# Kernel tuning notes

Hardware: AMD Instinct MI355X
Metric: run time of the kernel (lower is better)

Reference implementation:

```python
import math
import jax, jax.numpy as jnp
import numpy as np

NUM_HEADS = 16
NUM_LANDMARKS = 64
INV_ITERS = 6
ATT_SIZE = 1024
HEAD_SIZE = ATT_SIZE // NUM_HEADS  # dk = 64
NEG = -100000.0


def moore_penrose_pinv(x, num_iter):
    # lucidrains-style iterative Moore-Penrose pseudo-inverse
    abs_x = jnp.abs(x)
    col = abs_x.sum(axis=-1)
    row = abs_x.sum(axis=-2)
    z = jnp.swapaxes(x, -1, -2) / (jnp.max(col) * jnp.max(row))
    I = jnp.eye(x.shape[-1], dtype=x.dtype)
    for _ in range(num_iter):
        xz = x @ z
        z = 0.25 * z @ (13.0 * I - xz @ (15.0 * I - xz @ (7.0 * I - xz)))
    return z


def masked_softmax_scores(k, q, mask):
    # q @ k^T (dk=1: q already scaled) + mask, softmax over last dim
    s = jnp.einsum('bhmd,bhld->bhml', q, k)
    if mask is not None:
        s = s + (1.0 - mask) * NEG
    return jax.nn.softmax(s, axis=-1)


def setup_inputs() -> dict:
    key = jax.random.key(0)
    k1, k2, k3 = jax.random.split(key, 3)
    B, L, D = 4, 4096, 1024
    x = jax.random.normal(k1, (B, L, D), dtype=jnp.float32)
    attention_mask = jnp.ones((B, L), dtype=jnp.float32)
    w_kqv = jax.random.normal(k2, (3 * ATT_SIZE, D), dtype=jnp.float32) * 0.02
    w_out = jax.random.normal(k3, (ATT_SIZE, ATT_SIZE), dtype=jnp.float32) * 0.02
    b_out = jnp.zeros((ATT_SIZE,), dtype=jnp.float32)
    return {"x": x, "attention_mask": attention_mask,
            "w_kqv": w_kqv, "w_out": w_out, "b_out": b_out}


def reference(x, attention_mask, w_kqv, w_out, b_out):
    B, L, D = x.shape
    H, nl, hd = NUM_HEADS, NUM_LANDMARKS, HEAD_SIZE
    seg = L // nl  # landmark segment length (L already a multiple of nl)

    kqv = x @ w_kqv.T  # [B, L, 3A]
    k, q, v = jnp.split(kqv, 3, axis=-1)
    split = lambda t: t.reshape(B, L, H, hd).transpose(0, 2, 1, 3)  # [B,H,L,hd]
    k, q, v = split(k), split(q), split(v)

    mask = attention_mask[:, None, :]  # [B,1,L]
    denom = mask.reshape(B, 1, nl, seg).sum(-1) + 1e-08  # [B,1,nl]
    mask_lm = (denom > 0).astype(x.dtype)  # [B,1,nl]
    denom4 = denom[..., None]              # [B,1,nl,1]
    maskL = mask[..., None]                # [B,1,L,1]

    q = q * maskL
    k = k * maskL
    v = v * maskL

    s1_mask = maskL * mask_lm[..., None, :]               # [B,1,L,nl]
    s2_mask = mask_lm[..., None] * mask_lm[..., None, :]  # [B,1,nl,nl]
    s3_mask = jnp.swapaxes(s1_mask, -1, -2)               # [B,1,nl,L]

    q = q / math.sqrt(HEAD_SIZE)
    q_lm = q.reshape(B, H, nl, seg, hd).sum(-2) / denom4  # [B,H,nl,hd]
    k_lm = k.reshape(B, H, nl, seg, hd).sum(-2) / denom4

    scores_1 = masked_softmax_scores(k_lm, q, s1_mask)     # [B,H,L,nl]
    scores_2 = masked_softmax_scores(k_lm, q_lm, s2_mask)  # [B,H,nl,nl]
    scores_3 = masked_softmax_scores(k, q_lm, s3_mask)     # [B,H,nl,L]

    z_star = moore_penrose_pinv(scores_2, INV_ITERS)       # [B,H,nl,nl]
    out = scores_1 @ (z_star @ (scores_3 @ v))             # [B,H,L,hd]

    out = out.transpose(0, 2, 1, 3).reshape(B, L, H * hd)  # merge heads
    return out @ w_out.T + b_out
```

## Files before the change

kernel.cpp:

```cpp
#include <hip/hip_runtime.h>
#include <hip/hip_bf16.h>


static constexpr int Bn  = 4;
static constexpr int Ln  = 4096;
static constexpr int Dn  = 1024;
static constexpr int Hn  = 16;
static constexpr int HDn = 64;
static constexpr int NLn = 64;
static constexpr int SEGn = 64;
static constexpr int BHn = Bn * Hn;
static constexpr int Mn  = Bn * Ln;
static constexpr int NCH = 8;
#define NEG_BIG (-100000.0f)

static constexpr size_t OFF_KT  = 0;
static constexpr size_t OFF_QT  = 16777216;
static constexpr size_t OFF_VT  = 33554432;
static constexpr size_t OFF_WOH = 33554432;
static constexpr size_t OFF_WH  = 50331648;
static constexpr size_t OFF_QLM = 50331648;
static constexpr size_t OFF_KLM = 50593792;
static constexpr size_t OFF_S2  = 50855936;
static constexpr size_t OFF_Z   = 51118080;
static constexpr size_t OFF_WM  = 51380224;
static constexpr size_t OFF_PM  = 51642368;
static constexpr size_t OFF_PS  = 51675136;
static constexpr size_t OFF_GM  = 51707904;
static constexpr size_t OFF_XS  = 53477376;
static constexpr size_t OFF_PO  = 53477376;

using bf16x8 = __attribute__((ext_vector_type(8))) short;
using f32x16 = __attribute__((ext_vector_type(16))) float;
using s16x4  = __attribute__((ext_vector_type(4))) short;

__device__ __forceinline__ unsigned short f2bf(float f) {
    unsigned int u = __float_as_uint(f);
    return (unsigned short)((u + 0x7fffu + ((u >> 16) & 1u)) >> 16);
}
__device__ __forceinline__ float bf2f(unsigned short h) {
    return __uint_as_float((unsigned int)h << 16);
}
__device__ __forceinline__ void cvt8s(const float* fs, bf16x8& hv, bf16x8& lv) {
    #pragma unroll
    for (int e = 0; e < 8; ++e) {
        const unsigned int u = __float_as_uint(fs[e]);
        const unsigned short h = (unsigned short)(u >> 16);
        hv[e] = (short)h;
        lv[e] = (short)f2bf(fs[e] - bf2f(h));
    }
}
typedef __attribute__((address_space(1))) void gvoid;
typedef __attribute__((address_space(3))) void lvoid;
__device__ __forceinline__ void async16(void* l, const void* g) {
    __builtin_amdgcn_global_load_lds((gvoid*)(size_t)g, (lvoid*)l, 16, 0, 0);
}

__global__ __launch_bounds__(256) void k_pack(
    const float* __restrict__ src, unsigned short* __restrict__ dh, int row0)
{
    __shared__ float Ls[128][33];
    const int rt = blockIdx.x, kt = blockIdx.y;
    const int tid = threadIdx.x;
    #pragma unroll
    for (int p = 0; p < 4; ++p) {
        const int row = p * 32 + (tid >> 3);
        const int c4 = (tid & 7) * 4;
        const float4 v = *(const float4*)&src[(size_t)(row0 + rt * 128 + row) * 1024 + kt * 32 + c4];
        Ls[row][c4 + 0] = v.x; Ls[row][c4 + 1] = v.y;
        Ls[row][c4 + 2] = v.z; Ls[row][c4 + 3] = v.w;
    }
    __syncthreads();
    const size_t tb = (size_t)(rt * 32 + kt) * 4096;
    for (int s = tid; s < 512; s += 256) {
        const int g = s >> 7, kk = (s >> 6) & 1, l = s & 63;
        const int row = g * 32 + (l & 31);
        const int k0 = kk * 16 + ((l >> 5) & 1) * 8;
        bf16x8 hv;
        #pragma unroll
        for (int e = 0; e < 8; ++e) hv[e] = (short)f2bf(Ls[row][k0 + e]);
        *(bf16x8*)&dh[tb + s * 8] = hv;
    }
}

#define GEMM4W_CORE(A_, B_, NNB)                                               \
    __shared__ __attribute__((aligned(16))) char smem[16384];                  \
    const int tid = threadIdx.x;                                               \
    const int lane = tid & 63, wid = tid >> 6;                                 \
    const int cpx = gridDim.x >> 3;                                            \
    const int wg = (blockIdx.x & 7) * cpx + (blockIdx.x >> 3);                 \
    const int bm = wg / (NNB), bn = wg % (NNB);                                \
    const int wrow = wid >> 1, wcol = wid & 1;                                 \
    const unsigned short* gsrc =                                               \
        (wid < 2 ? (A_) + (size_t)bm * 131072 : (B_) + (size_t)bn * 131072)    \
        + (wid & 1) * 2048 + lane * 8;                                         \
    char* ldst = smem + wid * 4096;                                            \
    f32x16 acc[2][2] = {};                                                     \
    for (int kt = 0; kt < 32; ++kt) {                                          \
        const unsigned short* g = gsrc + (size_t)kt * 4096;                    \
        __syncthreads();                                                       \
        _Pragma("unroll")                                                      \
        for (int i = 0; i < 4; ++i)                                            \
            async16(ldst + i * 1024, g + i * 512);                             \
        __syncthreads();                                                       \
        _Pragma("unroll")                                                      \
        for (int kk = 0; kk < 2; ++kk) {                                       \
            bf16x8 fa[2], fb[2];                                               \
            _Pragma("unroll")                                                  \
            for (int ti = 0; ti < 2; ++ti) {                                   \
                const int o = (((wrow * 2 + ti) * 2 + kk) << 10) + lane * 16;  \
                fa[ti] = *(const bf16x8*)(smem + o);                           \
            }                                                                  \
            _Pragma("unroll")                                                  \
            for (int tj = 0; tj < 2; ++tj) {                                   \
                const int o = (((wcol * 2 + tj) * 2 + kk) << 10) + lane * 16;  \
                fb[tj] = *(const bf16x8*)(smem + 8192 + o);                    \
            }                                                                  \
            _Pragma("unroll")                                                  \
            for (int ti = 0; ti < 2; ++ti)                                     \
                _Pragma("unroll")                                              \
                for (int tj = 0; tj < 2; ++tj)                                 \
                    acc[ti][tj] = __builtin_amdgcn_mfma_f32_32x32x16_bf16(     \
                        fa[ti], fb[tj], acc[ti][tj], 0, 0, 0);                 \
        }                                                                      \
    }

__global__ __launch_bounds__(256) void k_kqv_gemm(
    const unsigned short* __restrict__ xh,
    const unsigned short* __restrict__ wh,
    const float* __restrict__ mask,
    float* __restrict__ Kt, float* __restrict__ Qt, float* __restrict__ Vt,
    int row0)
{
    GEMM4W_CORE(xh, wh, 24)
    const int part = bn >> 3;
    #pragma unroll
    for (int ti = 0; ti < 2; ++ti) {
        #pragma unroll
        for (int tj = 0; tj < 2; ++tj) {
            const int col = (bn * 128 + wcol * 64 + tj * 32 + (lane & 31)) & 1023;
            const int h = col >> 6, d = col & 63;
            #pragma unroll
            for (int r = 0; r < 16; ++r) {
                const int row = row0 + bm * 128 + wrow * 64 + ti * 32
                              + (r & 3) + 8 * (r >> 2) + 4 * (lane >> 5);
                const int b = row >> 12, l = row & 4095;
                const float mk = mask[b * Ln + l];
                const size_t idx = ((size_t)(b * Hn + h) * Ln + l) * HDn + d;
                const float v = acc[ti][tj][r] * mk;
                if (part == 0)      Kt[idx] = v;
                else if (part == 1) Qt[idx] = v * 0.125f;
                else                Vt[idx] = v;
            }
        }
    }
}

__global__ __launch_bounds__(256) void k_out_gemm(
    const unsigned short* __restrict__ ah_,
    const unsigned short* __restrict__ bh_,
    const float* __restrict__ bias, float* __restrict__ out)
{
    GEMM4W_CORE(ah_, bh_, 8)
    #pragma unroll
    for (int ti = 0; ti < 2; ++ti) {
        #pragma unroll
        for (int tj = 0; tj < 2; ++tj) {
            const int col = bn * 128 + wcol * 64 + tj * 32 + (lane & 31);
            const float bb = bias[col];
            #pragma unroll
            for (int r = 0; r < 16; ++r) {
                const int row = bm * 128 + wrow * 64 + ti * 32
                              + (r & 3) + 8 * (r >> 2) + 4 * (lane >> 5);
                out[(size_t)row * Dn + col] = acc[ti][tj][r] + bb;
            }
        }
    }
}

__global__ __launch_bounds__(64) void k_landmarks(
    const float* __restrict__ Kt, const float* __restrict__ Qt,
    const float* __restrict__ mask,
    float* __restrict__ klm, float* __restrict__ qlm, int* __restrict__ gmax)
{
    const int blk = blockIdx.x;
    const int m = blk & 63, bh = blk >> 6, b = bh >> 4;
    const int d = threadIdx.x;
    if (blk == 0 && d < 2) gmax[d] = 0;
    float mv = mask[b * Ln + m * SEGn + d];
    #pragma unroll
    for (int off = 32; off; off >>= 1) mv += __shfl_down(mv, off);
    const float denom = __shfl(mv, 0) + 1e-8f;
    const float* kp = Kt + ((size_t)bh * Ln + m * SEGn) * HDn + d;
    const float* qp = Qt + ((size_t)bh * Ln + m * SEGn) * HDn + d;
    float sk = 0.f, sq = 0.f;
    for (int j = 0; j < SEGn; ++j) {
        sk += kp[(size_t)j * HDn];
        sq += qp[(size_t)j * HDn];
    }
    klm[((size_t)bh * NLn + m) * HDn + d] = sk / denom;
    qlm[((size_t)bh * NLn + m) * HDn + d] = sq / denom;
}

__global__ __launch_bounds__(64) void k_s2(
    const float* __restrict__ qlm, const float* __restrict__ klm,
    float* __restrict__ s2, int* __restrict__ gmax)
{
    const int bh = blockIdx.x;
    __shared__ float ql[64][65];
    __shared__ float kl[64][65];
    __shared__ float sr[64][65];
    const int t = threadIdx.x;
    for (int idx = t; idx < 4096; idx += 64) {
        ql[idx >> 6][idx & 63] = qlm[(size_t)bh * 4096 + idx];
        kl[idx >> 6][idx & 63] = klm[(size_t)bh * 4096 + idx];
    }
    __syncthreads();
    float mx = -1e30f;
    for (int mp = 0; mp < 64; ++mp) {
        float s = 0.f;
        #pragma unroll 8
        for (int d2 = 0; d2 < 64; ++d2) s = fmaf(ql[t][d2], kl[mp][d2], s);
        sr[t][mp] = s;
        mx = fmaxf(mx, s);
    }
    float sum = 0.f;
    for (int mp = 0; mp < 64; ++mp) {
        const float e = expf(sr[t][mp] - mx);
        sr[t][mp] = e;
        sum += e;
    }
    const float inv = 1.f / sum;
    float rs = 0.f;
    for (int mp = 0; mp < 64; ++mp) {
        const float v = sr[t][mp] * inv;
        sr[t][mp] = v;
        s2[(size_t)bh * 4096 + t * 64 + mp] = v;
        rs += fabsf(v);
    }
    __syncthreads();
    float cs = 0.f;
    for (int mm = 0; mm < 64; ++mm) cs += fabsf(sr[mm][t]);
    float rmax = rs, cmax = cs;
    #pragma unroll
    for (int off = 32; off; off >>= 1) {
        rmax = fmaxf(rmax, __shfl_down(rmax, off));
        cmax = fmaxf(cmax, __shfl_down(cmax, off));
    }
    if (t == 0) {
        atomicMax(&gmax[0], __float_as_int(rmax));
        atomicMax(&gmax[1], __float_as_int(cmax));
    }
}

template<int SUB>
__device__ __forceinline__ void mm64v(
    float* C, int ldc, const float* Ag, int lda,
    const float* Bm, int ldb, float dg, float scl)
{
    const int tid = threadIdx.x;
    const int tx = tid & 15, ty = tid >> 4;
    const int i0 = ty << 2, j0 = tx << 2;
    float acc[4][4] = {};
    for (int k0 = 0; k0 < 64; k0 += 4) {
        float4 a4[4], b4[4];
        #pragma unroll
        for (int i = 0; i < 4; ++i)
            a4[i] = *(const float4*)&Ag[(size_t)(i0 + i) * lda + k0];
        #pragma unroll
        for (int kk = 0; kk < 4; ++kk)
            b4[kk] = *(const float4*)&Bm[(size_t)(k0 + kk) * ldb + j0];
        if (SUB) {
            #pragma unroll
            for (int kk = 0; kk < 4; ++kk) {
                float* bp = (float*)&b4[kk];
                #pragma unroll
                for (int j = 0; j < 4; ++j)
                    bp[j] = ((k0 + kk == j0 + j) ? dg : 0.0f) - bp[j];
            }
        }
        #pragma unroll
        for (int i = 0; i < 4; ++i) {
            const float* ap = (const float*)&a4[i];
            #pragma unroll
            for (int kk = 0; kk < 4; ++kk) {
                const float* bp = (const float*)&b4[kk];
                #pragma unroll
                for (int j = 0; j < 4; ++j)
                    acc[i][j] = fmaf(ap[kk], bp[j], acc[i][j]);
            }
        }
    }
    __syncthreads();
    #pragma unroll
    for (int i = 0; i < 4; ++i)
        #pragma unroll
        for (int j = 0; j < 4; ++j) C[(size_t)(i0 + i) * ldc + j0 + j] = scl * acc[i][j];
    __syncthreads();
}

__global__ __launch_bounds__(256) void k_pinv(
    const float* __restrict__ s2, const int* __restrict__ gmax,
    float* __restrict__ zout)
{
    __shared__ float Zb[64][68];
    __shared__ float XZ[64][68];
    __shared__ float Tb[64][68];
    const int bh = blockIdx.x;
    const int tid = threadIdx.x;
    const float* X = s2 + (size_t)bh * 4096;
    const float scale = 1.0f / (__int_as_float(gmax[0]) * __int_as_float(gmax[1]));
    for (int idx = tid; idx < 4096; idx += 256) {
        const int i = idx >> 6, j = idx & 63;
        Zb[i][j] = X[j * 64 + i] * scale;
    }
    __syncthreads();
    for (int it = 0; it < 6; ++it) {
        mm64v<0>(&XZ[0][0], 68, X, 64, &Zb[0][0], 68, 0.f, 1.f);
        mm64v<1>(&Tb[0][0], 68, &XZ[0][0], 68, &XZ[0][0], 68, 7.f, 1.f);
        mm64v<1>(&Tb[0][0], 68, &XZ[0][0], 68, &Tb[0][0], 68, 15.f, 1.f);
        mm64v<1>(&Zb[0][0], 68, &Zb[0][0], 68, &Tb[0][0], 68, 13.f, 0.25f);
    }
    for (int idx = tid; idx < 4096; idx += 256)
        zout[(size_t)bh * 4096 + idx] = Zb[idx >> 6][idx & 63];
}

__global__ __launch_bounds__(256) void k_s3v_part(
    const float* __restrict__ qlm, const float* __restrict__ Kt,
    const float* __restrict__ Vt, const float* __restrict__ mask,
    float* __restrict__ Opart, float* __restrict__ mpart, float* __restrict__ spart)
{
    __shared__ float Sm[64][65];
    __shared__ float Ks[64][65];
    __shared__ float Vs[64][65];
    __shared__ unsigned short Qp[2][4096];
    __shared__ float red[64][4], red2[64][4];
    __shared__ float rowmax[64], rowsum[64], fac[64], mrow[64];
    const int bh = blockIdx.x, ch = blockIdx.y;
    const int b = bh >> 4;
    const int tid = threadIdx.x;
    const int lane = tid & 63, wid = tid >> 6;
    const int wr = wid >> 1, wc = wid & 1;

    for (int idx = tid; idx < 4096; idx += 256)
        Sm[idx >> 6][idx & 63] = qlm[(size_t)bh * 4096 + idx];
    if (tid < 64) { rowmax[tid] = -1e30f; rowsum[tid] = 0.f; }
    __syncthreads();
    for (int s = tid; s < 512; s += 256) {
        const int g = s >> 8, kc = (s >> 6) & 3, l = s & 63;
        const int row = g * 32 + (l & 31);
        const int k0 = kc * 16 + ((l >> 5) & 1) * 8;
        bf16x8 hv, lv;
        cvt8s(&Sm[row][k0], hv, lv);
        *(bf16x8*)&Qp[0][s * 8] = hv;
        *(bf16x8*)&Qp[1][s * 8] = lv;
    }
    f32x16 accO = {};
    const int t0beg = ch * (Ln / NCH), t0end = t0beg + (Ln / NCH);
    for (int t0 = t0beg; t0 < t0end; t0 += 64) {
        __syncthreads();
        for (int idx = tid; idx < 4096; idx += 256) {
            const int r = idx >> 6, c2 = idx & 63;
            Ks[r][c2] = Kt[((size_t)bh * Ln + t0 + r) * HDn + c2];
            Vs[r][c2] = Vt[((size_t)bh * Ln + t0 + r) * HDn + c2];
        }
        if (tid < 64) mrow[tid] = mask[b * Ln + t0 + tid];
        __syncthreads();
        f32x16 acc = {};
        #pragma unroll
        for (int kc = 0; kc < 4; ++kc) {
            const bf16x8 a_h = *(const bf16x8*)&Qp[0][((wr * 4 + kc) * 64 + lane) * 8];
            const bf16x8 a_l = *(const bf16x8*)&Qp[1][((wr * 4 + kc) * 64 + lane) * 8];
            const int brow = wc * 32 + (lane & 31);
            const int k0 = kc * 16 + (lane >> 5) * 8;
            bf16x8 b_h, b_l;
            cvt8s(&Ks[brow][k0], b_h, b_l);
            acc = __builtin_amdgcn_mfma_f32_32x32x16_bf16(a_h, b_h, acc, 0, 0, 0);
            acc = __builtin_amdgcn_mfma_f32_32x32x16_bf16(a_h, b_l, acc, 0, 0, 0);
            acc = __builtin_amdgcn_mfma_f32_32x32x16_bf16(a_l, b_h, acc, 0, 0, 0);
        }
        #pragma unroll
        for (int r = 0; r < 16; ++r) {
            const int row = wr * 32 + (r & 3) + 8 * (r >> 2) + 4 * (lane >> 5);
            const int col = wc * 32 + (lane & 31);
            Sm[row][col] = acc[r] + (1.f - mrow[col]) * NEG_BIG;
        }
        __syncthreads();
        {
            const int row = tid >> 2, sg = tid & 3, c0 = sg * 16;
            float mx = -1e30f;
            #pragma unroll
            for (int c = 0; c < 16; ++c) mx = fmaxf(mx, Sm[row][c0 + c]);
            red[row][sg] = mx;
            __syncthreads();
            const float nm = fmaxf(rowmax[row],
                fmaxf(fmaxf(red[row][0], red[row][1]), fmaxf(red[row][2], red[row][3])));
            const float f = __expf(rowmax[row] - nm);
            float ps = 0.f;
            #pragma unroll
            for (int c = 0; c < 16; ++c) {
                const float e = __expf(Sm[row][c0 + c] - nm);
                Sm[row][c0 + c] = e;
                ps += e;
            }
            red2[row][sg] = ps;
            __syncthreads();
            if (sg == 0) {
                rowsum[row] = rowsum[row] * f
                    + red2[row][0] + red2[row][1] + red2[row][2] + red2[row][3];
                rowmax[row] = nm;
                fac[row] = f;
            }
        }
        __syncthreads();
        #pragma unroll
        for (int r = 0; r < 16; ++r) {
            const int row = wr * 32 + (r & 3) + 8 * (r >> 2) + 4 * (lane >> 5);
            accO[r] *= fac[row];
        }
        #pragma unroll
        for (int kc = 0; kc < 4; ++kc) {
            const int arow = wr * 32 + (lane & 31);
            const int ak0 = kc * 16 + (lane >> 5) * 8;
            bf16x8 a_h, a_l;
            cvt8s(&Sm[arow][ak0], a_h, a_l);
            const int bcol = wc * 32 + (lane & 31);
            const int bk0 = kc * 16 + (lane >> 5) * 8;
            float bw[8];
            #pragma unroll
            for (int e = 0; e < 8; ++e) bw[e] = Vs[bk0 + e][bcol];
            bf16x8 b_h, b_l;
            cvt8s(bw, b_h, b_l);
            accO = __builtin_amdgcn_mfma_f32_32x32x16_bf16(a_h, b_h, accO, 0, 0, 0);
            accO = __builtin_amdgcn_mfma_f32_32x32x16_bf16(a_h, b_l, accO, 0, 0, 0);
            accO = __builtin_amdgcn_mfma_f32_32x32x16_bf16(a_l, b_h, accO, 0, 0, 0);
        }
    }
    __syncthreads();
    #pragma unroll
    for (int r = 0; r < 16; ++r) {
        const int row = wr * 32 + (r & 3) + 8 * (r >> 2) + 4 * (lane >> 5);
        Vs[row][wc * 32 + (lane & 31)] = accO[r];
    }
    __syncthreads();
    const size_t ob = (size_t)(bh * NCH + ch) * 4096;
    for (int idx = tid; idx < 4096; idx += 256)
        Opart[ob + idx] = Vs[idx >> 6][idx & 63];
    if (tid < 64) {
        mpart[(bh * NCH + ch) * 64 + tid] = rowmax[tid];
        spart[(bh * NCH + ch) * 64 + tid] = rowsum[tid];
    }
}

__global__ __launch_bounds__(256) void k_mergez(
    const float* __restrict__ Opart, const float* __restrict__ mpart,
    const float* __restrict__ spart, const float* __restrict__ Zs,
    float* __restrict__ Wm)
{
    __shared__ float Sv[64][68];
    __shared__ float Zb[64][68];
    const int bh = blockIdx.x, tid = threadIdx.x;
    for (int idx = tid; idx < 4096; idx += 256)
        Zb[idx >> 6][idx & 63] = Zs[(size_t)bh * 4096 + idx];
    {
        const int r = tid >> 2, c0 = (tid & 3) * 16;
        float e[NCH];
        float M = -1e30f;
        #pragma unroll
        for (int c = 0; c < NCH; ++c) {
            e[c] = mpart[(bh * NCH + c) * 64 + r];
            M = fmaxf(M, e[c]);
        }
        float S = 0.f;
        #pragma unroll
        for (int c = 0; c < NCH; ++c) {
            e[c] = expf(e[c] - M);
            S += spart[(bh * NCH + c) * 64 + r] * e[c];
        }
        const float invS = 1.f / S;
        for (int col = c0; col < c0 + 16; ++col) {
            float o = 0.f;
            #pragma unroll
            for (int c = 0; c < NCH; ++c)
                o += Opart[(size_t)(bh * NCH + c) * 4096 + r * 64 + col] * e[c];
            Sv[r][col] = o * invS;
        }
    }
    __syncthreads();
    const int tx = tid & 15, ty = tid >> 4;
    const int i0 = ty << 2, j0 = tx << 2;
    float acc[4][4] = {};
    for (int k0 = 0; k0 < 64; k0 += 4) {
        float4 a4[4], b4[4];
        #pragma unroll
        for (int i = 0; i < 4; ++i)
            a4[i] = *(const float4*)&Zb[i0 + i][k0];
        #pragma unroll
        for (int kk = 0; kk < 4; ++kk)
            b4[kk] = *(const float4*)&Sv[k0 + kk][j0];
        #pragma unroll
        for (int i = 0; i < 4; ++i) {
            const float* ap = (const float*)&a4[i];
            #pragma unroll
            for (int kk = 0; kk < 4; ++kk) {
                const float* bp = (const float*)&b4[kk];
                #pragma unroll
                for (int j = 0; j < 4; ++j)
                    acc[i][j] = fmaf(ap[kk], bp[j], acc[i][j]);
            }
        }
    }
    #pragma unroll
    for (int i = 0; i < 4; ++i)
        #pragma unroll
        for (int j = 0; j < 4; ++j)
            Wm[(size_t)bh * 4096 + (i0 + i) * 64 + j0 + j] = acc[i][j];
}

__global__ __launch_bounds__(256) void k_attn_out(
    const float* __restrict__ Qt, const float* __restrict__ klm,
    const float* __restrict__ Wm, unsigned short* __restrict__ ah)
{
    const int lt = blockIdx.x;
    const int bh = blockIdx.y;
    const int b = bh >> 4, h = bh & 15;
    __shared__ float Sm[64][65];
    __shared__ float Ks[64][65];
    __shared__ float Ws[64][65];
    __shared__ unsigned short Qp[2][4096];
    __shared__ float red[64][4], red2[64][4];
    __shared__ float invr[64];
    const int tid = threadIdx.x;
    const int lane = tid & 63, wid = tid >> 6;
    const int wr = wid >> 1, wc = wid & 1;

    for (int idx = tid; idx < 4096; idx += 256) {
        const int r = idx >> 6, c2 = idx & 63;
        Sm[r][c2] = Qt[((size_t)bh * Ln + lt * 64 + r) * HDn + c2];
        Ks[r][c2] = klm[(size_t)bh * 4096 + idx];
        Ws[r][c2] = Wm[(size_t)bh * 4096 + idx];
    }
    __syncthreads();
    for (int s = tid; s < 512; s += 256) {
        const int g = s >> 8, kc = (s >> 6) & 3, l = s & 63;
        const int row = g * 32 + (l & 31);
        const int k0 = kc * 16 + ((l >> 5) & 1) * 8;
        bf16x8 hv, lv;
        cvt8s(&Sm[row][k0], hv, lv);
        *(bf16x8*)&Qp[0][s * 8] = hv;
        *(bf16x8*)&Qp[1][s * 8] = lv;
    }
    __syncthreads();
    f32x16 acc = {};
    #pragma unroll
    for (int kc = 0; kc < 4; ++kc) {
        const bf16x8 a_h = *(const bf16x8*)&Qp[0][((wr * 4 + kc) * 64 + lane) * 8];
        const bf16x8 a_l = *(const bf16x8*)&Qp[1][((wr * 4 + kc) * 64 + lane) * 8];
        const int brow = wc * 32 + (lane & 31);
        const int k0 = kc * 16 + (lane >> 5) * 8;
        bf16x8 b_h, b_l;
        cvt8s(&Ks[brow][k0], b_h, b_l);
        acc = __builtin_amdgcn_mfma_f32_32x32x16_bf16(a_h, b_h, acc, 0, 0, 0);
        acc = __builtin_amdgcn_mfma_f32_32x32x16_bf16(a_h, b_l, acc, 0, 0, 0);
        acc = __builtin_amdgcn_mfma_f32_32x32x16_bf16(a_l, b_h, acc, 0, 0, 0);
    }
    #pragma unroll
    for (int r = 0; r < 16; ++r) {
        const int row = wr * 32 + (r & 3) + 8 * (r >> 2) + 4 * (lane >> 5);
        Sm[row][wc * 32 + (lane & 31)] = acc[r];
    }
    __syncthreads();
    {
        const int row = tid >> 2, sg = tid & 3, c0 = sg * 16;
        float mx = -1e30f;
        #pragma unroll
        for (int c = 0; c < 16; ++c) mx = fmaxf(mx, Sm[row][c0 + c]);
        red[row][sg] = mx;
        __syncthreads();
        mx = fmaxf(fmaxf(red[row][0], red[row][1]), fmaxf(red[row][2], red[row][3]));
        float ps = 0.f;
        #pragma unroll
        for (int c = 0; c < 16; ++c) {
            const float e = __expf(Sm[row][c0 + c] - mx);
            Sm[row][c0 + c] = e;
            ps += e;
        }
        red2[row][sg] = ps;
        __syncthreads();
        if (sg == 0)
            invr[row] = 1.f / (red2[row][0] + red2[row][1] + red2[row][2] + red2[row][3]);
    }
    __syncthreads();
    f32x16 acc2 = {};
    #pragma unroll
    for (int kc = 0; kc < 4; ++kc) {
        const int arow = wr * 32 + (lane & 31);
        const int ak0 = kc * 16 + (lane >> 5) * 8;
        bf16x8 a_h, a_l;
        cvt8s(&Sm[arow][ak0], a_h, a_l);
        const int bcol = wc * 32 + (lane & 31);
        const int bk0 = kc * 16 + (lane >> 5) * 8;
        float bw[8];
        #pragma unroll
        for (int e = 0; e < 8; ++e) bw[e] = Ws[bk0 + e][bcol];
        bf16x8 b_h, b_l;
        cvt8s(bw, b_h, b_l);
        acc2 = __builtin_amdgcn_mfma_f32_32x32x16_bf16(a_h, b_h, acc2, 0, 0, 0);
        acc2 = __builtin_amdgcn_mfma_f32_32x32x16_bf16(a_h, b_l, acc2, 0, 0, 0);
        acc2 = __builtin_amdgcn_mfma_f32_32x32x16_bf16(a_l, b_h, acc2, 0, 0, 0);
    }
    __syncthreads();
    #pragma unroll
    for (int r = 0; r < 16; ++r) {
        const int row = wr * 32 + (r & 3) + 8 * (r >> 2) + 4 * (lane >> 5);
        Ks[row][wc * 32 + (lane & 31)] = acc2[r];
    }
    __syncthreads();
    const int tx = tid & 15, ty = tid >> 4;
    const int i0 = ty << 2, j0 = tx << 2;
    const int kd = h * 64 + j0;
    const int kt2 = kd >> 5, kc2 = kd & 31;
    const int kk2 = kc2 >> 4, half = (kc2 & 15) >> 3, e0 = kc2 & 7;
    #pragma unroll
    for (int i = 0; i < 4; ++i) {
        const float inv = invr[i0 + i];
        const int gm = b * Ln + lt * 64 + i0 + i;
        const int mt = gm >> 7, g2 = (gm & 127) >> 5, lrow = gm & 31;
        const size_t u = (size_t)(mt * 32 + kt2) * 4096
                       + (size_t)(((g2 * 2 + kk2) * 64 + half * 32 + lrow) * 8 + e0);
        s16x4 hv;
        #pragma unroll
        for (int j = 0; j < 4; ++j)
            hv[j] = (short)f2bf(Ks[i0 + i][j0 + j] * inv);
        *(s16x4*)&ah[u] = hv;
    }
}

extern "C" void kernel_launch(void* const* d_in, const int* in_sizes, int n_in,
                              void* d_out, int out_size, void* d_ws, size_t ws_size,
                              hipStream_t stream)
{
    (void)in_sizes; (void)n_in; (void)out_size;
    const float* x    = (const float*)d_in[0];
    const float* mask = (const float*)d_in[1];
    const float* wkqv = (const float*)d_in[2];
    const float* wout = (const float*)d_in[3];
    const float* bout = (const float*)d_in[4];
    float* out = (float*)d_out;
    float* ws  = (float*)d_ws;

    float* Kt   = ws + OFF_KT;
    float* Qt   = ws + OFF_QT;
    float* Vt   = ws + OFF_VT;
    float* qlm  = ws + OFF_QLM;
    float* klm  = ws + OFF_KLM;
    float* s2   = ws + OFF_S2;
    float* zst  = ws + OFF_Z;
    float* Wm   = ws + OFF_WM;
    int*   gmax = (int*)(ws + OFF_GM);
    float* mpart = ws + OFF_PM;
    float* spart = ws + OFF_PS;
    float* Opart = ws + OFF_PO;
    unsigned short* wh  = (unsigned short*)(ws + OFF_WH);
    unsigned short* woh = (unsigned short*)(ws + OFF_WOH);
    unsigned short* attn_h = (unsigned short*)(ws + OFF_KT);

    int S = 2048;
    if (ws_size >= (size_t)(OFF_XS + 8192 * 512) * 4) S = 8192;
    else if (ws_size >= (size_t)(OFF_XS + 2097152) * 4) S = 4096;
    unsigned short* xhs = (unsigned short*)(ws + OFF_XS);

    k_pack<<<dim3(24, 32), 256, 0, stream>>>(wkqv, wh, 0);
    for (int s = 0; s < Mn / S; ++s) {
        k_pack<<<dim3(S / 128, 32), 256, 0, stream>>>(x, xhs, s * S);
        k_kqv_gemm<<<(S / 128) * 24, 256, 0, stream>>>(
            xhs, wh, mask, Kt, Qt, Vt, s * S);
    }
    k_landmarks<<<BHn * NLn, 64, 0, stream>>>(Kt, Qt, mask, klm, qlm, gmax);
    k_s2<<<BHn, 64, 0, stream>>>(qlm, klm, s2, gmax);
    k_pinv<<<BHn, 256, 0, stream>>>(s2, gmax, zst);
    k_s3v_part<<<dim3(BHn, NCH), 256, 0, stream>>>(qlm, Kt, Vt, mask, Opart, mpart, spart);
    k_pack<<<dim3(8, 32), 256, 0, stream>>>(wout, woh, 0);
    k_mergez<<<BHn, 256, 0, stream>>>(Opart, mpart, spart, zst, Wm);
    k_attn_out<<<dim3(Ln / 64, BHn), 256, 0, stream>>>(Qt, klm, Wm, attn_h);
    k_out_gemm<<<128 * 8, 256, 0, stream>>>(attn_h, woh, bout, out);
}
```

Baseline: 461.1 us.

## Drop split-bf16 correction MFMAs, widen pinv to 512 threads, enlarge pack chunk

Replaces the three-MFMA hi/lo split-bf16 products in the s3v and attention-output kernels with a single rounded-bf16 MFMA, which removes two thirds of that matrix work and the low-part conversions and LDS staging. The pinv kernel now runs 512 threads per block, each computing a 2x4 tile instead of 4x4, to add parallelism to the serial Newton iterations. The x pack/GEMM chunk grows to 16384 rows when the workspace allows, cutting launches. Dropping the correction terms lowers accuracy in the softmax-weighted products.

```diff
diff --git a/kernel.cpp b/kernel.cpp
--- a/kernel.cpp
+++ b/kernel.cpp
@@ -38,17 +38,9 @@
     unsigned int u = __float_as_uint(f);
     return (unsigned short)((u + 0x7fffu + ((u >> 16) & 1u)) >> 16);
 }
-__device__ __forceinline__ float bf2f(unsigned short h) {
-    return __uint_as_float((unsigned int)h << 16);
-}
-__device__ __forceinline__ void cvt8s(const float* fs, bf16x8& hv, bf16x8& lv) {
-    #pragma unroll
-    for (int e = 0; e < 8; ++e) {
-        const unsigned int u = __float_as_uint(fs[e]);
-        const unsigned short h = (unsigned short)(u >> 16);
-        hv[e] = (short)h;
-        lv[e] = (short)f2bf(fs[e] - bf2f(h));
-    }
+__device__ __forceinline__ void cvt8r(const float* fs, bf16x8& hv) {
+    #pragma unroll
+    for (int e = 0; e < 8; ++e) hv[e] = (short)f2bf(fs[e]);
 }
 typedef __attribute__((address_space(1))) void gvoid;
 typedef __attribute__((address_space(3))) void lvoid;
@@ -77,8 +69,7 @@
         const int row = g * 32 + (l & 31);
         const int k0 = kk * 16 + ((l >> 5) & 1) * 8;
         bf16x8 hv;
-        #pragma unroll
-        for (int e = 0; e < 8; ++e) hv[e] = (short)f2bf(Ls[row][k0 + e]);
+        cvt8r(&Ls[row][k0], hv);
         *(bf16x8*)&dh[tb + s * 8] = hv;
     }
 }
@@ -254,18 +245,18 @@
 }
 
 template<int SUB>
-__device__ __forceinline__ void mm64v(
+__device__ __forceinline__ void mm64v512(
     float* C, int ldc, const float* Ag, int lda,
     const float* Bm, int ldb, float dg, float scl)
 {
     const int tid = threadIdx.x;
     const int tx = tid & 15, ty = tid >> 4;
-    const int i0 = ty << 2, j0 = tx << 2;
-    float acc[4][4] = {};
+    const int i0 = ty << 1, j0 = tx << 2;
+    float acc[2][4] = {};
     for (int k0 = 0; k0 < 64; k0 += 4) {
-        float4 a4[4], b4[4];
-        #pragma unroll
-        for (int i = 0; i < 4; ++i)
+        float4 a4[2], b4[4];
+        #pragma unroll
+        for (int i = 0; i < 2; ++i)
             a4[i] = *(const float4*)&Ag[(size_t)(i0 + i) * lda + k0];
         #pragma unroll
         for (int kk = 0; kk < 4; ++kk)
@@ -280,7 +271,7 @@
             }
         }
         #pragma unroll
-        for (int i = 0; i < 4; ++i) {
+        for (int i = 0; i < 2; ++i) {
             const float* ap = (const float*)&a4[i];
             #pragma unroll
             for (int kk = 0; kk < 4; ++kk) {
@@ -293,13 +284,13 @@
     }
     __syncthreads();
     #pragma unroll
-    for (int i = 0; i < 4; ++i)
+    for (int i = 0; i < 2; ++i)
         #pragma unroll
         for (int j = 0; j < 4; ++j) C[(size_t)(i0 + i) * ldc + j0 + j] = scl * acc[i][j];
     __syncthreads();
 }
 
-__global__ __launch_bounds__(256) void k_pinv(
+__global__ __launch_bounds__(512) void k_pinv(
     const float* __restrict__ s2, const int* __restrict__ gmax,
     float* __restrict__ zout)
 {
@@ -310,18 +301,18 @@
     const int tid = threadIdx.x;
     const float* X = s2 + (size_t)bh * 4096;
     const float scale = 1.0f / (__int_as_float(gmax[0]) * __int_as_float(gmax[1]));
-    for (int idx = tid; idx < 4096; idx += 256) {
+    for (int idx = tid; idx < 4096; idx += 512) {
         const int i = idx >> 6, j = idx & 63;
         Zb[i][j] = X[j * 64 + i] * scale;
     }
     __syncthreads();
     for (int it = 0; it < 6; ++it) {
-        mm64v<0>(&XZ[0][0], 68, X, 64, &Zb[0][0], 68, 0.f, 1.f);
-        mm64v<1>(&Tb[0][0], 68, &XZ[0][0], 68, &XZ[0][0], 68, 7.f, 1.f);
-        mm64v<1>(&Tb[0][0], 68, &XZ[0][0], 68, &Tb[0][0], 68, 15.f, 1.f);
-        mm64v<1>(&Zb[0][0], 68, &Zb[0][0], 68, &Tb[0][0], 68, 13.f, 0.25f);
-    }
-    for (int idx = tid; idx < 4096; idx += 256)
+        mm64v512<0>(&XZ[0][0], 68, X, 64, &Zb[0][0], 68, 0.f, 1.f);
+        mm64v512<1>(&Tb[0][0], 68, &XZ[0][0], 68, &XZ[0][0], 68, 7.f, 1.f);
+        mm64v512<1>(&Tb[0][0], 68, &XZ[0][0], 68, &Tb[0][0], 68, 15.f, 1.f);
+        mm64v512<1>(&Zb[0][0], 68, &Zb[0][0], 68, &Tb[0][0], 68, 13.f, 0.25f);
+    }
+    for (int idx = tid; idx < 4096; idx += 512)
         zout[(size_t)bh * 4096 + idx] = Zb[idx >> 6][idx & 63];
 }
 
@@ -333,7 +324,7 @@
     __shared__ float Sm[64][65];
     __shared__ float Ks[64][65];
     __shared__ float Vs[64][65];
-    __shared__ unsigned short Qp[2][4096];
+    __shared__ unsigned short Qp[4096];
     __shared__ float red[64][4], red2[64][4];
     __shared__ float rowmax[64], rowsum[64], fac[64], mrow[64];
     const int bh = blockIdx.x, ch = blockIdx.y;
@@ -350,10 +341,9 @@
         const int g = s >> 8, kc = (s >> 6) & 3, l = s & 63;
         const int row = g * 32 + (l & 31);
         const int k0 = kc * 16 + ((l >> 5) & 1) * 8;
-        bf16x8 hv, lv;
-        cvt8s(&Sm[row][k0], hv, lv);
-        *(bf16x8*)&Qp[0][s * 8] = hv;
-        *(bf16x8*)&Qp[1][s * 8] = lv;
+        bf16x8 hv;
+        cvt8r(&Sm[row][k0], hv);
+        *(bf16x8*)&Qp[s * 8] = hv;
     }
     f32x16 accO = {};
     const int t0beg = ch * (Ln / NCH), t0end = t0beg + (Ln / NCH);
@@ -369,15 +359,12 @@
         f32x16 acc = {};
         #pragma unroll
         for (int kc = 0; kc < 4; ++kc) {
-            const bf16x8 a_h = *(const bf16x8*)&Qp[0][((wr * 4 + kc) * 64 + lane) * 8];
-            const bf16x8 a_l = *(const bf16x8*)&Qp[1][((wr * 4 + kc) * 64 + lane) * 8];
+            const bf16x8 a_h = *(const bf16x8*)&Qp[((wr * 4 + kc) * 64 + lane) * 8];
             const int brow = wc * 32 + (lane & 31);
             const int k0 = kc * 16 + (lane >> 5) * 8;
-            bf16x8 b_h, b_l;
-            cvt8s(&Ks[brow][k0], b_h, b_l);
+            bf16x8 b_h;
+            cvt8r(&Ks[brow][k0], b_h);
             acc = __builtin_amdgcn_mfma_f32_32x32x16_bf16(a_h, b_h, acc, 0, 0, 0);
-            acc = __builtin_amdgcn_mfma_f32_32x32x16_bf16(a_h, b_l, acc, 0, 0, 0);
-            acc = __builtin_amdgcn_mfma_f32_32x32x16_bf16(a_l, b_h, acc, 0, 0, 0);
         }
         #pragma unroll
         for (int r = 0; r < 16; ++r) {
@@ -422,18 +409,16 @@
         for (int kc = 0; kc < 4; ++kc) {
             const int arow = wr * 32 + (lane & 31);
             const int ak0 = kc * 16 + (lane >> 5) * 8;
-            bf16x8 a_h, a_l;
-            cvt8s(&Sm[arow][ak0], a_h, a_l);
+            bf16x8 a_h;
+            cvt8r(&Sm[arow][ak0], a_h);
             const int bcol = wc * 32 + (lane & 31);
             const int bk0 = kc * 16 + (lane >> 5) * 8;
             float bw[8];
             #pragma unroll
             for (int e = 0; e < 8; ++e) bw[e] = Vs[bk0 + e][bcol];
-            bf16x8 b_h, b_l;
-            cvt8s(bw, b_h, b_l);
+            bf16x8 b_h;
+            cvt8r(bw, b_h);
             accO = __builtin_amdgcn_mfma_f32_32x32x16_bf16(a_h, b_h, accO, 0, 0, 0);
-            accO = __builtin_amdgcn_mfma_f32_32x32x16_bf16(a_h, b_l, accO, 0, 0, 0);
-            accO = __builtin_amdgcn_mfma_f32_32x32x16_bf16(a_l, b_h, accO, 0, 0, 0);
         }
     }
     __syncthreads();
@@ -527,7 +512,7 @@
     __shared__ float Sm[64][65];
     __shared__ float Ks[64][65];
     __shared__ float Ws[64][65];
-    __shared__ unsigned short Qp[2][4096];
+    __shared__ unsigned short Qp[4096];
     __shared__ float red[64][4], red2[64][4];
     __shared__ float invr[64];
     const int tid = threadIdx.x;
@@ -545,24 +530,20 @@
         const int g = s >> 8, kc = (s >> 6) & 3, l = s & 63;
         const int row = g * 32 + (l & 31);
         const int k0 = kc * 16 + ((l >> 5) & 1) * 8;
-        bf16x8 hv, lv;
-        cvt8s(&Sm[row][k0], hv, lv);
-        *(bf16x8*)&Qp[0][s * 8] = hv;
-        *(bf16x8*)&Qp[1][s * 8] = lv;
+        bf16x8 hv;
+        cvt8r(&Sm[row][k0], hv);
+        *(bf16x8*)&Qp[s * 8] = hv;
     }
     __syncthreads();
     f32x16 acc = {};
     #pragma unroll
     for (int kc = 0; kc < 4; ++kc) {
-        const bf16x8 a_h = *(const bf16x8*)&Qp[0][((wr * 4 + kc) * 64 + lane) * 8];
-        const bf16x8 a_l = *(const bf16x8*)&Qp[1][((wr * 4 + kc) * 64 + lane) * 8];
+        const bf16x8 a_h = *(const bf16x8*)&Qp[((wr * 4 + kc) * 64 + lane) * 8];
         const int brow = wc * 32 + (lane & 31);
         const int k0 = kc * 16 + (lane >> 5) * 8;
-        bf16x8 b_h, b_l;
-        cvt8s(&Ks[brow][k0], b_h, b_l);
+        bf16x8 b_h;
+        cvt8r(&Ks[brow][k0], b_h);
         acc = __builtin_amdgcn_mfma_f32_32x32x16_bf16(a_h, b_h, acc, 0, 0, 0);
-        acc = __builtin_amdgcn_mfma_f32_32x32x16_bf16(a_h, b_l, acc, 0, 0, 0);
-        acc = __builtin_amdgcn_mfma_f32_32x32x16_bf16(a_l, b_h, acc, 0, 0, 0);
     }
     #pragma unroll
     for (int r = 0; r < 16; ++r) {
@@ -596,18 +577,16 @@
     for (int kc = 0; kc < 4; ++kc) {
         const int arow = wr * 32 + (lane & 31);
         const int ak0 = kc * 16 + (lane >> 5) * 8;
-        bf16x8 a_h, a_l;
-        cvt8s(&Sm[arow][ak0], a_h, a_l);
+        bf16x8 a_h;
+        cvt8r(&Sm[arow][ak0], a_h);
         const int bcol = wc * 32 + (lane & 31);
         const int bk0 = kc * 16 + (lane >> 5) * 8;
         float bw[8];
         #pragma unroll
         for (int e = 0; e < 8; ++e) bw[e] = Ws[bk0 + e][bcol];
-        bf16x8 b_h, b_l;
-        cvt8s(bw, b_h, b_l);
+        bf16x8 b_h;
+        cvt8r(bw, b_h);
         acc2 = __builtin_amdgcn_mfma_f32_32x32x16_bf16(a_h, b_h, acc2, 0, 0, 0);
-        acc2 = __builtin_amdgcn_mfma_f32_32x32x16_bf16(a_h, b_l, acc2, 0, 0, 0);
-        acc2 = __builtin_amdgcn_mfma_f32_32x32x16_bf16(a_l, b_h, acc2, 0, 0, 0);
     }
     __syncthreads();
     #pragma unroll
@@ -666,7 +645,8 @@
     unsigned short* attn_h = (unsigned short*)(ws + OFF_KT);
 
     int S = 2048;
-    if (ws_size >= (size_t)(OFF_XS + 8192 * 512) * 4) S = 8192;
+    if (ws_size >= (size_t)(OFF_XS + 16384 * 512) * 4) S = 16384;
+    else if (ws_size >= (size_t)(OFF_XS + 8192 * 512) * 4) S = 8192;
     else if (ws_size >= (size_t)(OFF_XS + 2097152) * 4) S = 4096;
     unsigned short* xhs = (unsigned short*)(ws + OFF_XS);
 
@@ -678,7 +658,7 @@
     }
     k_landmarks<<<BHn * NLn, 64, 0, stream>>>(Kt, Qt, mask, klm, qlm, gmax);
     k_s2<<<BHn, 64, 0, stream>>>(qlm, klm, s2, gmax);
-    k_pinv<<<BHn, 256, 0, stream>>>(s2, gmax, zst);
+    k_pinv<<<BHn, 512, 0, stream>>>(s2, gmax, zst);
     k_s3v_part<<<dim3(BHn, NCH), 256, 0, stream>>>(qlm, Kt, Vt, mask, Opart, mpart, spart);
     k_pack<<<dim3(8, 32), 256, 0, stream>>>(wout, woh, 0);
     k_mergez<<<BHn, 256, 0, stream>>>(Opart, mpart, spart, zst, Wm);
```

Result: slower. 538.9 us (+16.9%).
